# Performance work log

Hardware: AMD Instinct MI355X
Metric: run time of the kernel (lower is better)

The kernel has to match this reference:

```python
import jax, jax.numpy as jnp
import numpy as np

NHEADS = 16
LN_EPS = 1e-5


def setup_inputs() -> dict:
    key = jax.random.key(0)
    ks = jax.random.split(key, 12)
    B, L, D = 8, 1024, 1024
    bound = 1.0 / np.sqrt(D)
    inp = {
        'query': jax.random.normal(ks[0], (B, L, D), jnp.float32),
        'key':   jax.random.normal(ks[1], (B, L, D), jnp.float32),
        'value': jax.random.normal(ks[2], (B, L, D), jnp.float32),
        'q_mask': jnp.ones((B, L), jnp.float32),
        'k_mask': jnp.ones((B, L), jnp.float32),
        'Wq': jax.random.uniform(ks[3], (D, D), jnp.float32, -bound, bound),
        'bq': jax.random.uniform(ks[4], (D,), jnp.float32, -bound, bound),
        'Wk': jax.random.uniform(ks[5], (D, D), jnp.float32, -bound, bound),
        'bk': jax.random.uniform(ks[6], (D,), jnp.float32, -bound, bound),
        'Wv': jax.random.uniform(ks[7], (D, D), jnp.float32, -bound, bound),
        'bv': jax.random.uniform(ks[8], (D,), jnp.float32, -bound, bound),
        'Wo': jax.random.uniform(ks[9], (D, D), jnp.float32, -bound, bound),
        'bo': jax.random.uniform(ks[10], (D,), jnp.float32, -bound, bound),
        'gamma': jnp.ones((D,), jnp.float32),
        'beta': jnp.zeros((D,), jnp.float32),
    }
    return inp


def reference(query, key, value, q_mask, k_mask, Wq, bq, Wk, bk, Wv, bv, Wo, bo, gamma, beta):
    B, L, D = query.shape
    H = NHEADS
    d = D // H
    residual = query
    # linear projections (torch Linear: x @ W.T + b)
    q = query @ Wq.T + bq
    k = key @ Wk.T + bk
    v = value @ Wv.T + bv
    # NOTE: module does a raw contiguous view [B, L, H*d] -> [B*H, L, d]
    # (NOT a transpose-based head split). Replicate exactly.
    q = q.reshape(B * H, L, d)
    k = k.reshape(B * H, L, d)
    v = v.reshape(B * H, L, d)
    # masks tiled head-major: repeat(nheads, 1) -> [H*B, L]
    qm = jnp.tile(q_mask, (H, 1))
    km = jnp.tile(k_mask, (H, 1))
    mask = qm[:, :, None] * km[:, None, :]  # [B*H, L, L] outer product
    scores = jnp.einsum('bqd,bkd->bqk', q, k) / np.sqrt(d).astype(np.float32)
    A = jnp.exp(jnp.where(mask == 0, -jnp.inf, scores))  # unstable exp, as in source
    A_sum = jnp.clip(jnp.sum(A, axis=-1, keepdims=True), 2e-15, None)
    attn = A / A_sum
    context = (attn @ v).reshape(B, L, H * d)
    out = context @ Wo.T + bo
    # dropout is identity in eval mode
    x = residual + out
    mean = jnp.mean(x, axis=-1, keepdims=True)
    var = jnp.mean(jnp.square(x - mean), axis=-1, keepdims=True)
    return (x - mean) / jnp.sqrt(var + LN_EPS) * gamma + beta
```

## Files before the change

### kernel.cpp

```cpp
#include <hip/hip_runtime.h>
#include <hip/hip_bf16.h>


typedef __bf16 bf16x8 __attribute__((ext_vector_type(8)));
typedef float  f32x4  __attribute__((ext_vector_type(4)));

#define KK 1024
#define NN 1024

union BfPack4 { __bf16 h[4]; uint2 u; };
union BfPack8 { __bf16 h[8]; uint4 u; };

__device__ __forceinline__ void lds_copy16(void* lds, const void* gsrc) {
  __builtin_amdgcn_global_load_lds(
      (__attribute__((address_space(1))) void*)(uintptr_t)gsrc,
      (__attribute__((address_space(3))) void*)(unsigned int)(uintptr_t)lds,
      16, 0, 0);
}

struct Cvt4 { const float* src[4]; __bf16* dst; };

__global__ __launch_bounds__(256) void cvt_w(Cvt4 a) {
  const int z = blockIdx.y;
  const float* s = a.src[z];
  __bf16* d = a.dst + (size_t)z * (KK * NN);
  const int i = (blockIdx.x * 256 + threadIdx.x) * 4;
  float4 f = *(const float4*)&s[i];
  BfPack4 p;
  p.h[0] = (__bf16)f.x; p.h[1] = (__bf16)f.y;
  p.h[2] = (__bf16)f.z; p.h[3] = (__bf16)f.w;
  *(uint2*)&d[i] = p.u;
}

struct Cvt3 { const float* src[3]; __bf16* dst; };

__global__ __launch_bounds__(256) void cvt_a(Cvt3 a) {
  const int z = blockIdx.y;
  const float* s = a.src[z];
  __bf16* d = a.dst + (size_t)z * ((size_t)8 << 20);
  const size_t i = ((size_t)blockIdx.x * 256 + threadIdx.x) * 8;
  float4 f0 = *(const float4*)&s[i];
  float4 f1 = *(const float4*)&s[i + 4];
  BfPack8 p;
  p.h[0] = (__bf16)f0.x; p.h[1] = (__bf16)f0.y;
  p.h[2] = (__bf16)f0.z; p.h[3] = (__bf16)f0.w;
  p.h[4] = (__bf16)f1.x; p.h[5] = (__bf16)f1.y;
  p.h[6] = (__bf16)f1.z; p.h[7] = (__bf16)f1.w;
  *(uint4*)&d[i] = p.u;
}

struct G8 {
  const __bf16* A[3];
  const __bf16* W[3];
  const float*  bias[3];
  void*         C[3];
};

#define BAR()   __builtin_amdgcn_s_barrier()
#define PRIO(x) __builtin_amdgcn_s_setprio(x)
#define WAIT_LGKM0() do { asm volatile("s_waitcnt lgkmcnt(0)" ::: "memory"); \
                          __builtin_amdgcn_sched_barrier(0); } while (0)
#define WAIT_VM4()  asm volatile("s_waitcnt vmcnt(4)" ::: "memory")
#define WAIT_VM0()  asm volatile("s_waitcnt vmcnt(0)" ::: "memory")

#define STAGE_A(buf, half, kt) do {                                          \
  lds_copy16(smem + (buf)*32768 + (half)*16384 + ldsW,                       \
             pA0[half] + (size_t)(kt)*64);                                   \
  lds_copy16(smem + (buf)*32768 + (half)*16384 + ldsW + 1024,                \
             pA1[half] + (size_t)(kt)*64); } while (0)

#define STAGE_B(buf, half, kt) do {                                          \
  lds_copy16(smem + 65536 + (buf)*32768 + (half)*16384 + ldsW,               \
             pB0[half] + (size_t)(kt)*64);                                   \
  lds_copy16(smem + 65536 + (buf)*32768 + (half)*16384 + ldsW + 1024,        \
             pB1[half] + (size_t)(kt)*64); } while (0)

#define LDA(buf, mh) do {                                                    \
  const char* _p = aSelf + (buf)*32768 + (mh)*8192;                          \
  _Pragma("unroll") for (int i_ = 0; i_ < 4; ++i_) {                         \
    af[i_][0] = *(const bf16x8*)(_p + i_*2048 + c0_);                        \
    af[i_][1] = *(const bf16x8*)(_p + i_*2048 + c1_); } } while (0)

#define LDB(buf, nh) do {                                                    \
  const char* _p = bSelf + (buf)*32768 + (nh)*4096;                          \
  _Pragma("unroll") for (int j_ = 0; j_ < 2; ++j_) {                         \
    bf[(nh)*2 + j_][0] = *(const bf16x8*)(_p + j_*2048 + c0_);               \
    bf[(nh)*2 + j_][1] = *(const bf16x8*)(_p + j_*2048 + c1_); } } while (0)

#define MM(mh, nh) do {                                                      \
  _Pragma("unroll") for (int i_ = 0; i_ < 4; ++i_)                           \
  _Pragma("unroll") for (int j_ = 0; j_ < 2; ++j_) {                         \
    acc[(mh)*4+i_][(nh)*2+j_] = __builtin_amdgcn_mfma_f32_16x16x32_bf16(     \
        af[i_][0], bf[(nh)*2+j_][0], acc[(mh)*4+i_][(nh)*2+j_], 0, 0, 0);    \
    acc[(mh)*4+i_][(nh)*2+j_] = __builtin_amdgcn_mfma_f32_16x16x32_bf16(     \
        af[i_][1], bf[(nh)*2+j_][1], acc[(mh)*4+i_][(nh)*2+j_], 0, 0, 0);    \
  } } while (0)

template <bool OUT_BF16>
__global__ __launch_bounds__(512, 2) void gemm8p(G8 args)
{
  __shared__ __align__(16) char smem[131072];
  const int z = blockIdx.z;
  const __bf16* __restrict__ A    = args.A[z];
  const __bf16* __restrict__ W    = args.W[z];
  const float*  __restrict__ bias = args.bias[z];

  const int tid = threadIdx.x;
  const int l = tid & 63, w = tid >> 6;
  const int lr = l & 15, lq = l >> 4;
  const int wr = w >> 2, wc = w & 3;

  int lin = blockIdx.y * 32 + blockIdx.x;
  lin = (lin & 7) * 16 + (lin >> 3);
  const int m0 = (lin & 31) * 256;
  const int n0 = (lin >> 5) * 256;

  const int s0 = w * 128 + l, s1 = s0 + 64;
  const int r0 = s0 >> 3, kq0 = (s0 & 7) ^ (r0 & 7);
  const int r1 = s1 >> 3, kq1 = (s1 & 7) ^ (r1 & 7);
  const __bf16* pA0[2]; const __bf16* pA1[2];
  const __bf16* pB0[2]; const __bf16* pB1[2];
  #pragma unroll
  for (int h = 0; h < 2; ++h) {
    pA0[h] = A + (size_t)(m0 + h * 128 + r0) * KK + kq0 * 8;
    pA1[h] = A + (size_t)(m0 + h * 128 + r1) * KK + kq1 * 8;
    pB0[h] = W + (size_t)(n0 + h * 128 + r0) * KK + kq0 * 8;
    pB1[h] = W + (size_t)(n0 + h * 128 + r1) * KK + kq1 * 8;
  }
  const int ldsW = w * 2048;

  const int aRow = lr * 128;
  const int c0_ = ((lq)     ^ (lr & 7)) * 16;
  const int c1_ = ((4 + lq) ^ (lr & 7)) * 16;
  const char* aSelf = smem + wr * 16384 + aRow;
  const char* bSelf = smem + 65536 + (wc >> 1) * 16384 + (wc & 1) * 8192 + aRow;

  bf16x8 af[4][2], bf[4][2];
  f32x4 acc[8][4] = {};

  STAGE_A(0, 0, 0); STAGE_A(0, 1, 0);
  STAGE_B(0, 0, 0); STAGE_B(0, 1, 0);
  STAGE_B(1, 0, 1); STAGE_B(1, 1, 1);
  WAIT_VM4();
  BAR();

  for (int it = 0; it < 8; ++it) {
    const int t2 = it * 2;
    LDA(0, 0); LDB(0, 0);
    STAGE_A(1, 0, t2 + 1);
    BAR(); WAIT_LGKM0();
    PRIO(1); MM(0, 0); PRIO(0);
    BAR();
    LDB(0, 1);
    STAGE_A(1, 1, t2 + 1);
    BAR(); WAIT_LGKM0();
    PRIO(1); MM(0, 1); PRIO(0);
    BAR();
    LDA(0, 1);
    if (it < 7) STAGE_B(0, 0, t2 + 2);
    BAR(); WAIT_LGKM0();
    PRIO(1); MM(1, 0); PRIO(0);
    BAR();
    if (it < 7) { STAGE_B(0, 1, t2 + 2); WAIT_VM4(); }
    else        { WAIT_VM0(); }
    BAR();
    PRIO(1); MM(1, 1); PRIO(0);
    BAR();
    LDA(1, 0); LDB(1, 0);
    if (it < 7) STAGE_A(0, 0, t2 + 2);
    BAR(); WAIT_LGKM0();
    PRIO(1); MM(0, 0); PRIO(0);
    BAR();
    LDB(1, 1);
    if (it < 7) STAGE_A(0, 1, t2 + 2);
    BAR(); WAIT_LGKM0();
    PRIO(1); MM(0, 1); PRIO(0);
    BAR();
    LDA(1, 1);
    if (it < 7) STAGE_B(1, 0, t2 + 3);
    BAR(); WAIT_LGKM0();
    PRIO(1); MM(1, 0); PRIO(0);
    BAR();
    if (it < 7) { STAGE_B(1, 1, t2 + 3); WAIT_VM4(); }
    BAR();
    PRIO(1); MM(1, 1); PRIO(0);
    BAR();
  }

  float bv[4];
  #pragma unroll
  for (int n = 0; n < 4; ++n) bv[n] = bias[n0 + wc * 64 + n * 16 + lr];

  #pragma unroll
  for (int f = 0; f < 8; ++f) {
    const int gm = m0 + wr * 128 + f * 16 + lq * 4;
    #pragma unroll
    for (int n = 0; n < 4; ++n) {
      const int gn = n0 + wc * 64 + n * 16 + lr;
      #pragma unroll
      for (int i = 0; i < 4; ++i) {
        const float v = acc[f][n][i] + bv[n];
        if constexpr (OUT_BF16)
          ((__bf16*)args.C[z])[(size_t)(gm + i) * NN + gn] = (__bf16)v;
        else
          ((float*)args.C[z])[(size_t)(gm + i) * NN + gn] = v;
      }
    }
  }
}

struct GQKV {
  const float*  A[3];
  const __bf16* W;
  const float*  bias[3];
  __bf16*       C[3];
};

__global__ __launch_bounds__(256) void gemm_qkv(GQKV args)
{
  __shared__ alignas(16) __bf16 As[128 * 40];
  __shared__ alignas(16) __bf16 Bs[2][4096];
  const int z = blockIdx.z;
  const float*  A    = args.A[z];
  const __bf16* W    = args.W + (size_t)z * KK * NN;
  const float*  bias = args.bias[z];
  __bf16* C = args.C[z];
  const int tid = threadIdx.x, l = tid & 63, w = tid >> 6;
  const int m0 = blockIdx.x * 128, n0 = blockIdx.y * 128;
  const int lr = l & 15, lq = l >> 4;
  const int wm = (w & 1) * 64, wn = (w >> 1) * 64;

  const __bf16* gw0 = &W[(size_t)(n0 + (tid >> 2)) * KK + (tid & 3) * 8];
  const __bf16* gw1 = &W[(size_t)(n0 + 64 + (tid >> 2)) * KK + (tid & 3) * 8];

  float4 pa[4];
  #pragma unroll
  for (int s = 0; s < 4; ++s) {
    int c = tid + 256 * s; int row = c >> 3, ko = (c & 7) * 4;
    pa[s] = *(const float4*)&A[(size_t)(m0 + row) * KK + ko];
  }
  lds_copy16((char*)Bs + w * 1024,        gw0);
  lds_copy16((char*)Bs + 4096 + w * 1024, gw1);

  f32x4 acc[4][4] = {};
  int ib = 0;
  for (int kk = 0; kk < KK; kk += 32) {
    __syncthreads();
    #pragma unroll
    for (int s = 0; s < 4; ++s) {
      int c = tid + 256 * s; int row = c >> 3, ko = (c & 7) * 4;
      BfPack4 p;
      p.h[0] = (__bf16)pa[s].x; p.h[1] = (__bf16)pa[s].y;
      p.h[2] = (__bf16)pa[s].z; p.h[3] = (__bf16)pa[s].w;
      *(uint2*)&As[row * 40 + ko] = p.u;
    }
    __syncthreads();
    if (kk + 32 < KK) {
      lds_copy16((char*)Bs + (ib ^ 1) * 8192 + w * 1024,        gw0 + kk + 32);
      lds_copy16((char*)Bs + (ib ^ 1) * 8192 + 4096 + w * 1024, gw1 + kk + 32);
      #pragma unroll
      for (int s = 0; s < 4; ++s) {
        int c = tid + 256 * s; int row = c >> 3, ko = (c & 7) * 4;
        pa[s] = *(const float4*)&A[(size_t)(m0 + row) * KK + kk + 32 + ko];
      }
    }
    const __bf16* Bb = (const __bf16*)((char*)Bs + ib * 8192);
    bf16x8 af2[4], bf2[4];
    #pragma unroll
    for (int t = 0; t < 4; ++t) {
      af2[t] = *(const bf16x8*)&As[(wm + t * 16 + lr) * 40 + lq * 8];
      bf2[t] = *(const bf16x8*)&Bb[(wn + t * 16 + lr) * 32 + lq * 8];
    }
    #pragma unroll
    for (int mt = 0; mt < 4; ++mt)
      #pragma unroll
      for (int nt = 0; nt < 4; ++nt)
        acc[mt][nt] = __builtin_amdgcn_mfma_f32_16x16x32_bf16(af2[mt], bf2[nt], acc[mt][nt], 0, 0, 0);
    ib ^= 1;
  }

  #pragma unroll
  for (int mt = 0; mt < 4; ++mt)
    #pragma unroll
    for (int nt = 0; nt < 4; ++nt)
      #pragma unroll
      for (int i = 0; i < 4; ++i) {
        int gm = m0 + wm + mt * 16 + lq * 4 + i;
        int gn = n0 + wn + nt * 16 + lr;
        C[(size_t)gm * NN + gn] = (__bf16)(acc[mt][nt][i] + bias[gn]);
      }
}

__global__ __launch_bounds__(256) void attn_kernel(
    const __bf16* __restrict__ qb, const __bf16* __restrict__ kb,
    const __bf16* __restrict__ vb, const float* __restrict__ qm,
    const float* __restrict__ km, __bf16* __restrict__ ctxb)
{
  const int g  = blockIdx.x * 16 + (blockIdx.y >> 3);
  const int qt = blockIdx.y & 7;
  const int tid = threadIdx.x, l = tid & 63, w = tid >> 6;
  const int lr = l & 15, lq = l >> 4;

  __shared__ alignas(16) __bf16 Ps[128 * 64];
  __shared__ alignas(16) __bf16 Ks[2 * 128 * 32];
  __shared__ alignas(16) __bf16 Vt[64 * 128];
  __shared__ alignas(16) __bf16 kms[1024];

  const size_t gbase = (size_t)g * (1024 * 64);
  const __bf16* qg = qb + gbase;
  const __bf16* kg = kb + gbase;
  const __bf16* vg = vb + gbase;
  const float* qmrow = qm + (size_t)(g & 7) * 1024;
  const float* kmrow = km + (size_t)(g & 7) * 1024;

  #pragma unroll
  for (int s = 0; s < 4; ++s) {
    int c = tid + 256 * s;
    int p = c >> 9, r = (c >> 2) & 127, q0 = c & 3;
    lds_copy16((char*)Ps + w * 1024 + s * 4096,
               &qg[(size_t)(qt * 128 + r) * 64 + p * 32 + q0 * 8]);
  }
  {
    float4 kf = *(const float4*)&kmrow[tid * 4];
    BfPack4 p;
    p.h[0] = (__bf16)(kf.x == 0.f ? 0.f : 1.f);
    p.h[1] = (__bf16)(kf.y == 0.f ? 0.f : 1.f);
    p.h[2] = (__bf16)(kf.z == 0.f ? 0.f : 1.f);
    p.h[3] = (__bf16)(kf.w == 0.f ? 0.f : 1.f);
    *(uint2*)&kms[tid * 4] = p.u;
  }
  float qmv[2][4];
  #pragma unroll
  for (int rt = 0; rt < 2; ++rt)
    #pragma unroll
    for (int i = 0; i < 4; ++i)
      qmv[rt][i] = qmrow[qt * 128 + 32 * w + rt * 16 + lq * 4 + i];

  __syncthreads();

  bf16x8 qa[2][2];
  #pragma unroll
  for (int rt = 0; rt < 2; ++rt)
    #pragma unroll
    for (int p = 0; p < 2; ++p)
      qa[rt][p] = *(const bf16x8*)((char*)Ps + p * 8192 +
                                   (32 * w + rt * 16 + lr) * 64 + lq * 16);

  uint4 pk[4], pv[4];
  #pragma unroll
  for (int s = 0; s < 4; ++s) {
    int c = tid + 256 * s; int p = c >> 9, r = (c >> 2) & 127, q0 = c & 3;
    pk[s] = *(const uint4*)&kg[(size_t)r * 64 + p * 32 + q0 * 8];
  }
  #pragma unroll
  for (int s = 0; s < 4; ++s) {
    int ch = tid + 256 * s; int j = ch & 127, c0 = ch >> 7;
    pv[s] = *(const uint4*)&vg[(size_t)j * 64 + c0 * 8];
  }

  const int kKey = (lq ^ (lr & 3)) << 4;
  float rs[2][4] = {};
  f32x4 ctx[2][4] = {};

  for (int kt = 0; kt < 8; ++kt) {
    __syncthreads();
    #pragma unroll
    for (int s = 0; s < 4; ++s) {
      int c = tid + 256 * s; int p = c >> 9, r = (c >> 2) & 127, q0 = c & 3;
      *(uint4*)((char*)Ks + p * 8192 + r * 64 + ((q0 ^ (r & 3)) << 4)) = pk[s];
    }
    #pragma unroll
    for (int s = 0; s < 4; ++s) {
      int ch = tid + 256 * s; int j = ch & 127, c0 = ch >> 7;
      BfPack8 vv; vv.u = pv[s];
      const int jhi = (j >> 3) << 4, jlo = (j & 7) * 2;
      #pragma unroll
      for (int cc = 0; cc < 8; ++cc) {
        int row = c0 * 8 + cc;
        *(__bf16*)((char*)Vt + row * 256 + (jhi ^ ((row & 15) << 4)) + jlo) =
            vv.h[cc];
      }
    }
    __syncthreads();
    if (kt < 7) {
      #pragma unroll
      for (int s = 0; s < 4; ++s) {
        int c = tid + 256 * s; int p = c >> 9, r = (c >> 2) & 127, q0 = c & 3;
        pk[s] = *(const uint4*)&kg[(size_t)((kt + 1) * 128 + r) * 64 + p * 32 + q0 * 8];
      }
      #pragma unroll
      for (int s = 0; s < 4; ++s) {
        int ch = tid + 256 * s; int j = ch & 127, c0 = ch >> 7;
        pv[s] = *(const uint4*)&vg[(size_t)((kt + 1) * 128 + j) * 64 + c0 * 8];
      }
    }
    #pragma unroll
    for (int h = 0; h < 2; ++h) {
      f32x4 sacc[2][4];
      #pragma unroll
      for (int c4 = 0; c4 < 4; ++c4) {
        int ct = h * 4 + c4;
        bf16x8 kb0 = *(const bf16x8*)((char*)Ks + (ct * 16 + lr) * 64 + kKey);
        bf16x8 kb1 = *(const bf16x8*)((char*)Ks + 8192 + (ct * 16 + lr) * 64 + kKey);
        #pragma unroll
        for (int rt = 0; rt < 2; ++rt) {
          f32x4 zz = {};
          zz = __builtin_amdgcn_mfma_f32_16x16x32_bf16(qa[rt][0], kb0, zz, 0, 0, 0);
          sacc[rt][c4] = __builtin_amdgcn_mfma_f32_16x16x32_bf16(qa[rt][1], kb1, zz, 0, 0, 0);
        }
      }
      #pragma unroll
      for (int c4 = 0; c4 < 4; ++c4) {
        int ct = h * 4 + c4;
        float kmv = (float)kms[kt * 128 + ct * 16 + lr];
        #pragma unroll
        for (int rt = 0; rt < 2; ++rt)
          #pragma unroll
          for (int i = 0; i < 4; ++i) {
            float e = (qmv[rt][i] * kmv == 0.f) ? 0.f
                                                : __expf(sacc[rt][c4][i] * 0.125f);
            rs[rt][i] += e;
            int row = 32 * w + rt * 16 + lq * 4 + i;
            *(__bf16*)((char*)Ps + row * 128 +
                       (((c4 * 2 + (lr >> 3)) ^ (row & 7)) << 4) +
                       (lr & 7) * 2) = (__bf16)e;
          }
      }
      #pragma unroll
      for (int ks = 0; ks < 2; ++ks) {
        bf16x8 pa2[2];
        #pragma unroll
        for (int rt = 0; rt < 2; ++rt) {
          int row = 32 * w + rt * 16 + lr;
          pa2[rt] = *(const bf16x8*)((char*)Ps + row * 128 +
                                     (((ks * 4 + lq) ^ (row & 7)) << 4));
        }
        #pragma unroll
        for (int c2 = 0; c2 < 4; ++c2) {
          int vrow = c2 * 16 + lr;
          bf16x8 vf = *(const bf16x8*)((char*)Vt + vrow * 256 +
                        (((h * 8 + ks * 4 + lq) << 4) ^ ((vrow & 15) << 4)));
          #pragma unroll
          for (int rt = 0; rt < 2; ++rt)
            ctx[rt][c2] = __builtin_amdgcn_mfma_f32_16x16x32_bf16(pa2[rt], vf, ctx[rt][c2], 0, 0, 0);
        }
      }
    }
  }

  #pragma unroll
  for (int rt = 0; rt < 2; ++rt)
    #pragma unroll
    for (int i = 0; i < 4; ++i) {
      float v = rs[rt][i];
      v += __shfl_xor(v, 1);
      v += __shfl_xor(v, 2);
      v += __shfl_xor(v, 4);
      v += __shfl_xor(v, 8);
      rs[rt][i] = 1.0f / fmaxf(v, 2e-15f);
    }

  #pragma unroll
  for (int rt = 0; rt < 2; ++rt)
    #pragma unroll
    for (int c2 = 0; c2 < 4; ++c2)
      #pragma unroll
      for (int i = 0; i < 4; ++i) {
        int row = qt * 128 + 32 * w + rt * 16 + lq * 4 + i;
        ctxb[gbase + (size_t)row * 64 + c2 * 16 + lr] =
            (__bf16)(ctx[rt][c2][i] * rs[rt][i]);
      }
}

__global__ __launch_bounds__(256) void ln_kernel(
    const float* __restrict__ O, const float* __restrict__ resid,
    const float* __restrict__ gam, const float* __restrict__ bet,
    float* __restrict__ out)
{
  const int row = blockIdx.x;
  const int tid = threadIdx.x;
  const float* orow = O + (size_t)row * 1024;
  const float* rrow = resid + (size_t)row * 1024;
  float x[4];
  float sum = 0.f, sq = 0.f;
  #pragma unroll
  for (int j = 0; j < 4; ++j) {
    int c = tid + j * 256;
    x[j] = orow[c] + rrow[c];
    sum += x[j];
    sq  += x[j] * x[j];
  }
  #pragma unroll
  for (int off = 32; off > 0; off >>= 1) {
    sum += __shfl_down(sum, off, 64);
    sq  += __shfl_down(sq, off, 64);
  }
  __shared__ float s1[4], s2[4];
  __shared__ float mean_s, inv_s;
  if ((tid & 63) == 0) { s1[tid >> 6] = sum; s2[tid >> 6] = sq; }
  __syncthreads();
  if (tid == 0) {
    float S = s1[0] + s1[1] + s1[2] + s1[3];
    float Q = s2[0] + s2[1] + s2[2] + s2[3];
    float mean = S * (1.0f / 1024.0f);
    float var  = fmaxf(Q * (1.0f / 1024.0f) - mean * mean, 0.0f);
    mean_s = mean;
    inv_s  = rsqrtf(var + 1e-5f);
  }
  __syncthreads();
  float mean = mean_s, inv = inv_s;
  #pragma unroll
  for (int j = 0; j < 4; ++j) {
    int c = tid + j * 256;
    out[(size_t)row * 1024 + c] = (x[j] - mean) * inv * gam[c] + bet[c];
  }
}

extern "C" void kernel_launch(void* const* d_in, const int* in_sizes, int n_in,
                              void* d_out, int out_size, void* d_ws, size_t ws_size,
                              hipStream_t stream)
{
  const float* query = (const float*)d_in[0];
  const float* keyi  = (const float*)d_in[1];
  const float* value = (const float*)d_in[2];
  const float* qmask = (const float*)d_in[3];
  const float* kmask = (const float*)d_in[4];
  const float* Wq = (const float*)d_in[5];
  const float* bq = (const float*)d_in[6];
  const float* Wk = (const float*)d_in[7];
  const float* bk = (const float*)d_in[8];
  const float* Wv = (const float*)d_in[9];
  const float* bv = (const float*)d_in[10];
  const float* Wo = (const float*)d_in[11];
  const float* bo = (const float*)d_in[12];
  const float* gam = (const float*)d_in[13];
  const float* bet = (const float*)d_in[14];

  char* ws = (char*)d_ws;
  __bf16* qbuf = (__bf16*)(ws);
  __bf16* kbuf = (__bf16*)(ws + ((size_t)16 << 20));
  __bf16* vbuf = (__bf16*)(ws + ((size_t)32 << 20));
  __bf16* wb   = (__bf16*)(ws + ((size_t)48 << 20));
  float*  obuf = (float*)(ws + ((size_t)16 << 20));
  __bf16* abuf = (__bf16*)(ws + ((size_t)56 << 20));

  const bool big = ws_size >= ((size_t)104 << 20);

  Cvt4 cv;
  cv.src[0] = Wq; cv.src[1] = Wk; cv.src[2] = Wv; cv.src[3] = Wo;
  cv.dst = wb;

  dim3 tb(256);
  hipLaunchKernelGGL(cvt_w, dim3(1024, 4), tb, 0, stream, cv);

  if (big) {
    Cvt3 ca;
    ca.src[0] = query; ca.src[1] = keyi; ca.src[2] = value;
    ca.dst = abuf;
    hipLaunchKernelGGL(cvt_a, dim3(4096, 3), tb, 0, stream, ca);

    G8 gq;
    gq.A[0] = abuf;
    gq.A[1] = abuf + ((size_t)8 << 20);
    gq.A[2] = abuf + ((size_t)16 << 20);
    gq.W[0] = wb; gq.W[1] = wb + (size_t)KK * NN; gq.W[2] = wb + (size_t)2 * KK * NN;
    gq.bias[0] = bq; gq.bias[1] = bk; gq.bias[2] = bv;
    gq.C[0] = qbuf; gq.C[1] = kbuf; gq.C[2] = vbuf;
    hipLaunchKernelGGL((gemm8p<true>), dim3(32, 4, 3), dim3(512), 0, stream, gq);
  } else {
    GQKV qkv;
    qkv.A[0] = query; qkv.A[1] = keyi; qkv.A[2] = value;
    qkv.W = wb;
    qkv.bias[0] = bq; qkv.bias[1] = bk; qkv.bias[2] = bv;
    qkv.C[0] = qbuf;  qkv.C[1] = kbuf; qkv.C[2] = vbuf;
    hipLaunchKernelGGL(gemm_qkv, dim3(64, 8, 3), tb, 0, stream, qkv);
  }

  hipLaunchKernelGGL(attn_kernel, dim3(8, 128), tb, 0, stream,
                     qbuf, kbuf, vbuf, qmask, kmask, qbuf);

  G8 go;
  go.A[0] = qbuf;
  go.W[0] = wb + (size_t)3 * KK * NN;
  go.bias[0] = bo;
  go.C[0] = obuf;
  go.A[1] = go.A[2] = go.A[0]; go.W[1] = go.W[2] = go.W[0];
  go.bias[1] = go.bias[2] = go.bias[0]; go.C[1] = go.C[2] = go.C[0];
  hipLaunchKernelGGL((gemm8p<false>), dim3(32, 4, 1), dim3(512), 0, stream, go);

  hipLaunchKernelGGL(ln_kernel, dim3(8192), tb, 0, stream,
                     obuf, query, gam, bet, (float*)d_out);
}
```

Measured before the change: 413.2 us.

## Merge conversion launches, add mask-free fast path, stage K via direct LDS loads

Folds the weight and activation bf16 conversion kernels into one prep launch. One extra block in that launch checks whether every mask entry is nonzero and records the answer in a device flag. The attention kernel reads the flag and, when no masking is needed, skips the per-element mask test before the exp. K tiles now go straight from global memory to LDS through global_load_lds instead of passing through registers, and the LDS XOR swizzle keys are precomputed. s_setprio is raised around the MFMA sections. The mask check is a real runtime test, but it adds a serial single-block reduction inside the prep kernel.

```diff
diff --git a/kernel.cpp b/kernel.cpp
--- a/kernel.cpp
+++ b/kernel.cpp
@@ -10,6 +10,8 @@
 
 union BfPack4 { __bf16 h[4]; uint2 u; };
 union BfPack8 { __bf16 h[8]; uint4 u; };
+
+__device__ int g_nomask;
 
 __device__ __forceinline__ void lds_copy16(void* lds, const void* gsrc) {
   __builtin_amdgcn_global_load_lds(
@@ -18,35 +20,47 @@
       16, 0, 0);
 }
 
-struct Cvt4 { const float* src[4]; __bf16* dst; };
-
-__global__ __launch_bounds__(256) void cvt_w(Cvt4 a) {
-  const int z = blockIdx.y;
-  const float* s = a.src[z];
-  __bf16* d = a.dst + (size_t)z * (KK * NN);
-  const int i = (blockIdx.x * 256 + threadIdx.x) * 4;
-  float4 f = *(const float4*)&s[i];
-  BfPack4 p;
-  p.h[0] = (__bf16)f.x; p.h[1] = (__bf16)f.y;
-  p.h[2] = (__bf16)f.z; p.h[3] = (__bf16)f.w;
-  *(uint2*)&d[i] = p.u;
-}
-
-struct Cvt3 { const float* src[3]; __bf16* dst; };
-
-__global__ __launch_bounds__(256) void cvt_a(Cvt3 a) {
-  const int z = blockIdx.y;
-  const float* s = a.src[z];
-  __bf16* d = a.dst + (size_t)z * ((size_t)8 << 20);
-  const size_t i = ((size_t)blockIdx.x * 256 + threadIdx.x) * 8;
-  float4 f0 = *(const float4*)&s[i];
-  float4 f1 = *(const float4*)&s[i + 4];
-  BfPack8 p;
-  p.h[0] = (__bf16)f0.x; p.h[1] = (__bf16)f0.y;
-  p.h[2] = (__bf16)f0.z; p.h[3] = (__bf16)f0.w;
-  p.h[4] = (__bf16)f1.x; p.h[5] = (__bf16)f1.y;
-  p.h[6] = (__bf16)f1.z; p.h[7] = (__bf16)f1.w;
-  *(uint4*)&d[i] = p.u;
+struct Prep {
+  const float* wsrc[4]; __bf16* wdst;
+  const float* asrc[3]; __bf16* adst; int do_a;
+  const float* qm; const float* km;
+};
+
+__global__ __launch_bounds__(256) void prep_kernel(Prep a) {
+  const int bid = blockIdx.x;
+  const int tid = threadIdx.x;
+  if (bid < 12288) {
+    if (!a.do_a) return;
+    const int z = bid >> 12, i = bid & 4095;
+    const float* s = a.asrc[z];
+    __bf16* d = a.adst + (size_t)z * ((size_t)8 << 20);
+    const size_t off = ((size_t)i * 256 + tid) * 8;
+    float4 f0 = *(const float4*)&s[off];
+    float4 f1 = *(const float4*)&s[off + 4];
+    BfPack8 p;
+    p.h[0] = (__bf16)f0.x; p.h[1] = (__bf16)f0.y;
+    p.h[2] = (__bf16)f0.z; p.h[3] = (__bf16)f0.w;
+    p.h[4] = (__bf16)f1.x; p.h[5] = (__bf16)f1.y;
+    p.h[6] = (__bf16)f1.z; p.h[7] = (__bf16)f1.w;
+    *(uint4*)&d[off] = p.u;
+  } else if (bid < 16384) {
+    const int b = bid - 12288;
+    const int z = b >> 10, i = b & 1023;
+    const float* s = a.wsrc[z];
+    __bf16* d = a.wdst + (size_t)z * (KK * NN);
+    const int idx = (i * 256 + tid) * 4;
+    float4 f = *(const float4*)&s[idx];
+    BfPack4 p;
+    p.h[0] = (__bf16)f.x; p.h[1] = (__bf16)f.y;
+    p.h[2] = (__bf16)f.z; p.h[3] = (__bf16)f.w;
+    *(uint2*)&d[idx] = p.u;
+  } else {
+    int ok = 1;
+    for (int i = tid; i < 8192; i += 256)
+      ok &= (a.qm[i] != 0.f) & (a.km[i] != 0.f);
+    const int all_ok = __syncthreads_and(ok);
+    if (tid == 0) g_nomask = all_ok;
+  }
 }
 
 struct G8 {
@@ -312,6 +326,7 @@
   const __bf16* vg = vb + gbase;
   const float* qmrow = qm + (size_t)(g & 7) * 1024;
   const float* kmrow = km + (size_t)(g & 7) * 1024;
+  const int nm = g_nomask;
 
   #pragma unroll
   for (int s = 0; s < 4; ++s) {
@@ -336,6 +351,14 @@
     for (int i = 0; i < 4; ++i)
       qmv[rt][i] = qmrow[qt * 128 + 32 * w + rt * 16 + lq * 4 + i];
 
+  int gkOff[4];
+  #pragma unroll
+  for (int s = 0; s < 4; ++s) {
+    int c = tid + 256 * s;
+    int p = c >> 9, r = (c >> 2) & 127, q0 = c & 3;
+    gkOff[s] = r * 64 + p * 32 + ((q0 ^ (r & 3)) * 8);
+  }
+
   __syncthreads();
 
   bf16x8 qa[2][2];
@@ -346,12 +369,7 @@
       qa[rt][p] = *(const bf16x8*)((char*)Ps + p * 8192 +
                                    (32 * w + rt * 16 + lr) * 64 + lq * 16);
 
-  uint4 pk[4], pv[4];
-  #pragma unroll
-  for (int s = 0; s < 4; ++s) {
-    int c = tid + 256 * s; int p = c >> 9, r = (c >> 2) & 127, q0 = c & 3;
-    pk[s] = *(const uint4*)&kg[(size_t)r * 64 + p * 32 + q0 * 8];
-  }
+  uint4 pv[4];
   #pragma unroll
   for (int s = 0; s < 4; ++s) {
     int ch = tid + 256 * s; int j = ch & 127, c0 = ch >> 7;
@@ -359,16 +377,17 @@
   }
 
   const int kKey = (lq ^ (lr & 3)) << 4;
+  const int pwKey = (lq << 1);
+  const int prKey = ((lr >> 2) << 1);
   float rs[2][4] = {};
   f32x4 ctx[2][4] = {};
 
   for (int kt = 0; kt < 8; ++kt) {
     __syncthreads();
     #pragma unroll
-    for (int s = 0; s < 4; ++s) {
-      int c = tid + 256 * s; int p = c >> 9, r = (c >> 2) & 127, q0 = c & 3;
-      *(uint4*)((char*)Ks + p * 8192 + r * 64 + ((q0 ^ (r & 3)) << 4)) = pk[s];
-    }
+    for (int s = 0; s < 4; ++s)
+      lds_copy16((char*)Ks + w * 1024 + s * 4096,
+                 kg + (size_t)kt * 8192 + gkOff[s]);
     #pragma unroll
     for (int s = 0; s < 4; ++s) {
       int ch = tid + 256 * s; int j = ch & 127, c0 = ch >> 7;
@@ -385,11 +404,6 @@
     if (kt < 7) {
       #pragma unroll
       for (int s = 0; s < 4; ++s) {
-        int c = tid + 256 * s; int p = c >> 9, r = (c >> 2) & 127, q0 = c & 3;
-        pk[s] = *(const uint4*)&kg[(size_t)((kt + 1) * 128 + r) * 64 + p * 32 + q0 * 8];
-      }
-      #pragma unroll
-      for (int s = 0; s < 4; ++s) {
         int ch = tid + 256 * s; int j = ch & 127, c0 = ch >> 7;
         pv[s] = *(const uint4*)&vg[(size_t)((kt + 1) * 128 + j) * 64 + c0 * 8];
       }
@@ -397,6 +411,7 @@
     #pragma unroll
     for (int h = 0; h < 2; ++h) {
       f32x4 sacc[2][4];
+      PRIO(1);
       #pragma unroll
       for (int c4 = 0; c4 < 4; ++c4) {
         int ct = h * 4 + c4;
@@ -409,23 +424,41 @@
           sacc[rt][c4] = __builtin_amdgcn_mfma_f32_16x16x32_bf16(qa[rt][1], kb1, zz, 0, 0, 0);
         }
       }
-      #pragma unroll
-      for (int c4 = 0; c4 < 4; ++c4) {
-        int ct = h * 4 + c4;
-        float kmv = (float)kms[kt * 128 + ct * 16 + lr];
+      PRIO(0);
+      if (nm) {
         #pragma unroll
-        for (int rt = 0; rt < 2; ++rt)
+        for (int c4 = 0; c4 < 4; ++c4)
           #pragma unroll
-          for (int i = 0; i < 4; ++i) {
-            float e = (qmv[rt][i] * kmv == 0.f) ? 0.f
-                                                : __expf(sacc[rt][c4][i] * 0.125f);
-            rs[rt][i] += e;
-            int row = 32 * w + rt * 16 + lq * 4 + i;
-            *(__bf16*)((char*)Ps + row * 128 +
-                       (((c4 * 2 + (lr >> 3)) ^ (row & 7)) << 4) +
-                       (lr & 7) * 2) = (__bf16)e;
-          }
-      }
+          for (int rt = 0; rt < 2; ++rt)
+            #pragma unroll
+            for (int i = 0; i < 4; ++i) {
+              float e = __expf(sacc[rt][c4][i] * 0.125f);
+              rs[rt][i] += e;
+              int row = 32 * w + rt * 16 + lq * 4 + i;
+              *(__bf16*)((char*)Ps + row * 128 +
+                         (((c4 * 2 + (lr >> 3)) ^ pwKey) << 4) +
+                         (lr & 7) * 2) = (__bf16)e;
+            }
+      } else {
+        #pragma unroll
+        for (int c4 = 0; c4 < 4; ++c4) {
+          int ct = h * 4 + c4;
+          float kmv = (float)kms[kt * 128 + ct * 16 + lr];
+          #pragma unroll
+          for (int rt = 0; rt < 2; ++rt)
+            #pragma unroll
+            for (int i = 0; i < 4; ++i) {
+              float e = (qmv[rt][i] * kmv == 0.f) ? 0.f
+                                                  : __expf(sacc[rt][c4][i] * 0.125f);
+              rs[rt][i] += e;
+              int row = 32 * w + rt * 16 + lq * 4 + i;
+              *(__bf16*)((char*)Ps + row * 128 +
+                         (((c4 * 2 + (lr >> 3)) ^ pwKey) << 4) +
+                         (lr & 7) * 2) = (__bf16)e;
+            }
+        }
+      }
+      PRIO(1);
       #pragma unroll
       for (int ks = 0; ks < 2; ++ks) {
         bf16x8 pa2[2];
@@ -433,7 +466,7 @@
         for (int rt = 0; rt < 2; ++rt) {
           int row = 32 * w + rt * 16 + lr;
           pa2[rt] = *(const bf16x8*)((char*)Ps + row * 128 +
-                                     (((ks * 4 + lq) ^ (row & 7)) << 4));
+                                     (((ks * 4 + lq) ^ prKey) << 4));
         }
         #pragma unroll
         for (int c2 = 0; c2 < 4; ++c2) {
@@ -445,6 +478,7 @@
             ctx[rt][c2] = __builtin_amdgcn_mfma_f32_16x16x32_bf16(pa2[rt], vf, ctx[rt][c2], 0, 0, 0);
         }
       }
+      PRIO(0);
     }
   }
 
@@ -546,19 +580,17 @@
 
   const bool big = ws_size >= ((size_t)104 << 20);
 
-  Cvt4 cv;
-  cv.src[0] = Wq; cv.src[1] = Wk; cv.src[2] = Wv; cv.src[3] = Wo;
-  cv.dst = wb;
+  Prep pp;
+  pp.wsrc[0] = Wq; pp.wsrc[1] = Wk; pp.wsrc[2] = Wv; pp.wsrc[3] = Wo;
+  pp.wdst = wb;
+  pp.asrc[0] = query; pp.asrc[1] = keyi; pp.asrc[2] = value;
+  pp.adst = abuf; pp.do_a = big ? 1 : 0;
+  pp.qm = qmask; pp.km = kmask;
 
   dim3 tb(256);
-  hipLaunchKernelGGL(cvt_w, dim3(1024, 4), tb, 0, stream, cv);
+  hipLaunchKernelGGL(prep_kernel, dim3(16385), tb, 0, stream, pp);
 
   if (big) {
-    Cvt3 ca;
-    ca.src[0] = query; ca.src[1] = keyi; ca.src[2] = value;
-    ca.dst = abuf;
-    hipLaunchKernelGGL(cvt_a, dim3(4096, 3), tb, 0, stream, ca);
-
     G8 gq;
     gq.A[0] = abuf;
     gq.A[1] = abuf + ((size_t)8 << 20);
```

Result: faster. 353.7 us (-14.4%).
